# Performance work log

Measured on AMD Instinct MI355X. Metric: run time of the kernel, lower is better.

## Reference

```python
import jax, jax.numpy as jnp
import numpy as np

ETA = 0.1
BETA = 0.1
MU = 0.1
PI_INIT = 0.7
MINI = 1e-6
C_TOTAL = 1e7  # corpus-level token count C[guided_m] (constant scale factor)


def setup_inputs() -> dict:
    key = jax.random.key(0)
    k1, k2, k3, k4, k5, k6 = jax.random.split(key, 6)
    B, V, K, D = 64, 8000, 50, 10000
    batch_BOW = jax.random.randint(k1, (B, V), 0, 3, dtype=jnp.int32)
    batch_indices = jax.random.randint(k2, (B,), 0, D)
    seeds_topic_matrix = (jax.random.uniform(k3, (V, K)) < 0.005).astype(jnp.float32)
    exp_m = jax.random.uniform(k4, (D, K)) * 10.0
    exp_n = jax.random.uniform(k5, (V, K)) * 5.0
    exp_s = jax.random.uniform(k6, (V, K)) * 2.0
    pi = jnp.full((K,), PI_INIT, dtype=jnp.float32)
    return {"batch_BOW": batch_BOW, "batch_indices": batch_indices,
            "seeds_topic_matrix": seeds_topic_matrix, "exp_m": exp_m,
            "exp_n": exp_n, "exp_s": exp_s, "pi": pi, "iter_n": 3}


def reference(batch_BOW, batch_indices, seeds_topic_matrix, exp_m, exp_n, exp_s, pi, iter_n):
    V, K = exp_n.shape
    beta_sum = BETA * V
    seed_word = seeds_topic_matrix.sum(axis=1) > 0          # [V] words that seed any topic
    S = seed_word.astype(exp_s.dtype).sum()
    mu_sum = MU * S
    exp_n_sum = exp_n.sum(axis=0)                            # [K]
    exp_s_sum = exp_s.sum(axis=0)                            # [K]

    bow = batch_BOW.astype(exp_m.dtype)                      # [B,V]
    mask = (bow > 0).astype(exp_m.dtype)[:, :, None]         # [B,V,1] BOW_nonzero gather
    theta = exp_m[batch_indices] + ETA                       # [B,K]

    seed_topic_term = ((MU + exp_s) / (mu_sum + exp_s_sum))[None]       # [1,V,K]
    reg_topic_term = ((BETA + exp_n) / (beta_sum + exp_n_sum))[None]    # [1,V,K]
    seeds_b = seeds_topic_matrix[None]                                   # [1,V,K]
    theta_b = theta[:, None, :]                                          # [B,1,K]

    gamma_ss = mask * seeds_b * theta_b * seed_topic_term * pi
    gamma_sr = mask * seeds_b * theta_b * reg_topic_term * (1.0 - pi)
    gamma_rr = mask * (1.0 - seeds_b) * theta_b * reg_topic_term

    s_sum = (gamma_ss + gamma_sr).sum(-1, keepdims=True)
    r_sum = gamma_rr.sum(-1, keepdims=True)
    gamma_ss = gamma_ss / (s_sum + MINI)
    gamma_sr = gamma_sr / (s_sum + MINI)
    gamma_rr = gamma_rr / (r_sum + MINI)

    # seed words use the mixture; non-seed words use regular-regular responsibilities
    gamma = jnp.where(seed_word[None, :, None],
                      pi * gamma_ss + (1.0 - pi) * (gamma_sr + gamma_rr),
                      gamma_rr)

    temp_exp_m = jnp.einsum('bvk,bv->bk', gamma, bow)
    temp_exp_n = jnp.einsum('bvk,bv->vk', gamma_sr + gamma_rr, bow)
    temp_exp_s = jnp.einsum('bvk,bv->vk', gamma_ss, bow)
    gamma_sr_sum = gamma_sr.sum(axis=(0, 1))
    exp_q_z = jnp.sum(gamma * jnp.log(gamma + MINI))

    rho = 1.0 / float((iter_n + 5) ** 0.9)
    batch_C = bow.sum()
    scale = C_TOTAL / batch_C

    exp_m_batch_new = (1.0 - rho) * exp_m[batch_indices] + rho * temp_exp_m
    exp_s_new = (1.0 - rho) * exp_s + rho * temp_exp_s * scale
    exp_n_new = (1.0 - rho) * exp_n + rho * temp_exp_n * scale

    exp_s_sum_new = exp_s_new.sum(axis=0)
    pi_new = exp_s_sum_new / (exp_s_sum_new + gamma_sr_sum + MINI)
    pi_new = jnp.where(pi_new > 0.1, pi_new, PI_INIT)

    return exp_m_batch_new, exp_n_new, exp_s_new, pi_new, exp_q_z
```

## Files before the change

kernel.cpp:

```cpp
#include <hip/hip_runtime.h>
#include <math.h>

constexpr int Bc = 64;
constexpr int Vc = 8000;
constexpr int Kc = 50;

#define WS_NSUM   0
#define WS_SSUM   50
#define WS_BATCHC 151
#define WS_SCNT   152
#define WS_QZSH   160
#define WS_PM     256
#define WS_GSRSH  51456
#define WS_SSNSH  54656
#define WS_ZEND   56256
#define WS_TH     56256
#define WS_SW     59456
#define WS_END    67456

#define FB_QZ     150
#define FB_GSR    200
#define FB_SSN    256

__global__ __launch_bounds__(256) void k1_pre(const int* __restrict__ bow,
    const float* __restrict__ seeds, const float* __restrict__ exp_n,
    const float* __restrict__ exp_s, const int* __restrict__ bidx,
    const float* __restrict__ exp_m, float* __restrict__ ws)
{
    const int t = threadIdx.x, blk = blockIdx.x;
    if (blk < 100) {
        __shared__ float csn[Kc], css[Kc];
        if (t < Kc) { csn[t] = 0.f; css[t] = 0.f; }
        __syncthreads();
        const int l = t & 63, w = t >> 6;
        const int q = (blk >> 1)*64 + l;
        const int k = q % 50;
        float sn = 0.f, ss = 0.f;
        for (int j = w + (blk & 1)*4; j < 125; j += 8) {
            int flat = j*3200 + q;
            sn += exp_n[flat];
            ss += exp_s[flat];
        }
        atomicAdd(&csn[k], sn);
        atomicAdd(&css[k], ss);
        __syncthreads();
        if (t < Kc) {
            atomicAdd(&ws[WS_NSUM + t], csn[t]);
            atomicAdd(&ws[WS_SSUM + t], css[t]);
        }
    } else if (blk < 164) {
        const int4* b4 = (const int4*)bow;
        int acc = 0;
        for (int i = (blk-100)*256 + t; i < Bc*Vc/4; i += 64*256) {
            int4 x = b4[i];
            acc += x.x + x.y + x.z + x.w;
        }
        for (int off = 32; off; off >>= 1) acc += __shfl_xor(acc, off);
        __shared__ int ri[4];
        if ((t & 63) == 0) ri[t >> 6] = acc;
        __syncthreads();
        if (t == 0) atomicAdd((int*)ws + WS_BATCHC, ri[0]+ri[1]+ri[2]+ri[3]);
    } else if (blk < 196) {
        int v = (blk-164)*256 + t;
        int any = 0;
        if (v < Vc) {
            const float2* rp = (const float2*)(seeds + v*Kc);
            for (int j = 0; j < 25; ++j) {
                float2 x = rp[j];
                any |= (x.x != 0.f) | (x.y != 0.f);
            }
            ws[WS_SW + v] = any ? 1.f : 0.f;
        }
        unsigned long long m = __ballot(any);
        if ((t & 63) == 0) atomicAdd((int*)ws + WS_SCNT, (int)__popcll(m));
    } else {
        for (int i = t; i < Bc*Kc; i += 256) {
            int b = i / Kc, k = i - b*Kc;
            ws[WS_TH + i] = exp_m[bidx[b]*Kc + k] + 0.1f;
        }
    }
}

__global__ __launch_bounds__(256) void kF(const int* __restrict__ bow,
    const float* __restrict__ seeds, const float* __restrict__ exp_n,
    const float* __restrict__ exp_s, const float* __restrict__ pi,
    const int* __restrict__ itern_p, float* __restrict__ ws,
    float* __restrict__ out)
{
    const int id = blockIdx.x;
    const int vt = (id & 7)*63 + (id >> 3);
    if (vt >= Vc/16) return;
    const int v0 = vt * 16;

    __shared__ float  th_l[64*51];
    __shared__ float  pmb[64*51];
    __shared__ float2 cd_l[16*50];
    __shared__ float2 gg_l[16*50];
    __shared__ float  n1_l[16*50];
    __shared__ float2 ii_l[16*64];
    __shared__ unsigned short bow_l[16*64];
    __shared__ float  den_l[152];
    __shared__ float  sw_l[16];
    __shared__ float  qz_l;

    const int t = threadIdx.x, lane = t & 63, w = t >> 6;

    int ii = itern_p[0];
    float itern = (ii >= 0 && ii < 1000000) ? (float)ii : __int_as_float(ii);
    const float rho = 1.f / powf(itern + 5.f, 0.9f);
    const float omr = 1.f - rho;

    for (int i = t; i < Bc*Kc; i += 256) {
        int b = i / 50, k = i - b*50;
        th_l[b*51 + k] = ws[WS_TH + i];
        pmb[b*51 + k]  = 0.f;
    }
    if (t < 50) {
        float Sf = (float)(((const int*)ws)[WS_SCNT]);
        den_l[t] = 1.f / (0.1f*Sf + ws[WS_SSUM + t]);
    } else if (t < 100) {
        den_l[t] = 1.f / (0.1f*(float)Vc + ws[WS_NSUM + t - 50]);
    } else if (t < 150) {
        den_l[t] = pi[t - 100];
    } else if (t >= 160 && t < 176) {
        sw_l[t - 160] = ws[WS_SW + v0 + (t - 160)];
    }
    for (int e = t; e < 16*64; e += 256) {
        int b = e >> 4, vl = e & 15;
        bow_l[vl*64 + b] = (unsigned short)bow[b*Vc + v0 + vl];
    }
    if (t == 0) qz_l = 0.f;
    __syncthreads();

    for (int i = t; i < 16*50; i += 256) {
        int vl = i / 50, k = i - vl*50;
        int g = v0*50 + i;
        float sv = seeds[g], en = exp_n[g], es = exp_s[g];
        float pk = den_l[100 + k];
        float st = (0.1f + es) * den_l[k];
        float rt = (0.1f + en) * den_l[50 + k];
        float sc = sv*st*pk;
        float n1 = sv*rt*(1.f - pk);
        float n2 = (1.f - sv)*rt;
        cd_l[i] = make_float2(sc + n1, n2);
        float ge = fmaf(pk, sc, (1.f - pk)*n1);
        float gf = (sw_l[vl] != 0.f) ? (1.f - pk)*n2 : n2;
        gg_l[i] = make_float2(ge, gf);
        n1_l[i] = n1;
    }
    __syncthreads();

    {
        float pm[Kc];
#pragma unroll
        for (int k = 0; k < Kc; ++k) pm[k] = 0.f;
        float qzacc0 = 0.f, qzacc1 = 0.f;

#pragma unroll 1
        for (int jj = 0; jj < 4; ++jj) {
            const int vl = w*4 + jj;
            const float bw = (float)bow_l[vl*64 + lane];
            const float4* cd4 = (const float4*)(cd_l + vl*50);
            float S = 0.f, S2 = 0.f, R = 0.f, R2 = 0.f;
#pragma unroll 5
            for (int k2 = 0; k2 < 25; ++k2) {
                float th0 = th_l[lane*51 + 2*k2];
                float th1 = th_l[lane*51 + 2*k2 + 1];
                float4 q = cd4[k2];
                S  = fmaf(th0, q.x, S);  R  = fmaf(th0, q.y, R);
                S2 = fmaf(th1, q.z, S2); R2 = fmaf(th1, q.w, R2);
            }
            S += S2; R += R2;
            const bool msk = bw > 0.f;
            const float is = msk ? 1.f/(S + 1e-6f) : 0.f;
            const float ir = msk ? 1.f/(R + 1e-6f) : 0.f;
            ii_l[vl*64 + lane] = make_float2(is, ir);
            const float4* gg4 = (const float4*)(gg_l + vl*50);
#pragma unroll
            for (int k2 = 0; k2 < 25; ++k2) {
                float th0 = th_l[lane*51 + 2*k2];
                float th1 = th_l[lane*51 + 2*k2 + 1];
                float4 q = gg4[k2];
                float t1a = fmaf(q.x, is, q.y*ir);
                float t1b = fmaf(q.z, is, q.w*ir);
                float ga = th0*t1a;
                float gb = th1*t1b;
                qzacc0 = fmaf(ga, __logf(ga + 1e-6f), qzacc0);
                qzacc1 = fmaf(gb, __logf(gb + 1e-6f), qzacc1);
                pm[2*k2]   = fmaf(bw, t1a, pm[2*k2]);
                pm[2*k2+1] = fmaf(bw, t1b, pm[2*k2+1]);
            }
        }

        float qz = qzacc0 + qzacc1;
        for (int off = 32; off; off >>= 1) qz += __shfl_xor(qz, off);
        if (lane == 0) atomicAdd(&qz_l, qz);

        for (int ww = 0; ww < 4; ++ww) {
            if (w == ww) {
#pragma unroll
                for (int k = 0; k < Kc; ++k) pmb[lane*51 + k] += pm[k];
            }
            __syncthreads();
        }
    }

    const int psh = (id & 7)*2 + ((id >> 3) & 1);
    for (int i = t; i < Bc*Kc; i += 256) {
        int b = i / 50, k = i - b*50;
        atomicAdd(&ws[WS_PM + psh*3200 + i], pmb[b*51 + k]);
    }
    if (t == 0) atomicAdd(&ws[WS_QZSH + (id & 31)], qz_l);

    {
        const float bC = (float)(((const int*)ws)[WS_BATCHC]);
        const float rs = rho * (1e7f / bC);
        float PT0=0.f,PT1=0.f,PT2=0.f,PT3=0.f;
        float QT0=0.f,QT1=0.f,QT2=0.f,QT3=0.f;
        float P20=0.f,P21=0.f,P22=0.f,P23=0.f;
#pragma unroll 8
        for (int b = 0; b < Bc; ++b) {
            float thv = th_l[b*51 + lane];
            float2 u0 = ii_l[(w*4+0)*64 + b];
            float2 u1 = ii_l[(w*4+1)*64 + b];
            float2 u2 = ii_l[(w*4+2)*64 + b];
            float2 u3 = ii_l[(w*4+3)*64 + b];
            float b0 = (float)bow_l[(w*4+0)*64 + b];
            float b1 = (float)bow_l[(w*4+1)*64 + b];
            float b2 = (float)bow_l[(w*4+2)*64 + b];
            float b3 = (float)bow_l[(w*4+3)*64 + b];
            PT0 = fmaf(b0*u0.x, thv, PT0); QT0 = fmaf(b0*u0.y, thv, QT0); P20 = fmaf(u0.x, thv, P20);
            PT1 = fmaf(b1*u1.x, thv, PT1); QT1 = fmaf(b1*u1.y, thv, QT1); P21 = fmaf(u1.x, thv, P21);
            PT2 = fmaf(b2*u2.x, thv, PT2); QT2 = fmaf(b2*u2.y, thv, QT2); P22 = fmaf(u2.x, thv, P22);
            PT3 = fmaf(b3*u3.x, thv, PT3); QT3 = fmaf(b3*u3.y, thv, QT3); P23 = fmaf(u3.x, thv, P23);
        }
        if (lane < Kc) {
            float PT[4] = {PT0, PT1, PT2, PT3};
            float QT[4] = {QT0, QT1, QT2, QT3};
            float P2[4] = {P20, P21, P22, P23};
            float gacc = 0.f, ssn = 0.f;
#pragma unroll
            for (int jj = 0; jj < 4; ++jj) {
                const int vl = w*4 + jj;
                const int li = vl*50 + lane;
                const int g  = (v0 + vl)*50 + lane;
                float n1v = n1_l[li];
                float2 cdv = cd_l[li];
                float tn  = fmaf(n1v, PT[jj], cdv.y*QT[jj]);
                float tsv = (cdv.x - n1v)*PT[jj];
                out[3200 + g]          = fmaf(omr, exp_n[g], rs*tn);
                float snew             = fmaf(omr, exp_s[g], rs*tsv);
                out[3200 + 400000 + g] = snew;
                gacc = fmaf(n1v, P2[jj], gacc);
                ssn += snew;
            }
            atomicAdd(&ws[WS_GSRSH + (id & 63)*Kc + lane], gacc);
            atomicAdd(&ws[WS_SSNSH + (id & 31)*Kc + lane], ssn);
        }
    }
}

__global__ __launch_bounds__(256) void kEnd(const int* __restrict__ itern_p,
    float* __restrict__ out, float* __restrict__ ws)
{
    const int t = threadIdx.x, blk = blockIdx.x;
    int ii = itern_p[0];
    float itern = (ii >= 0 && ii < 1000000) ? (float)ii : __int_as_float(ii);
    const float rho = 1.f / powf(itern + 5.f, 0.9f);
    const float omr = 1.f - rho;

    if (blk < 13) {
        int i = blk*256 + t;
        if (i < Bc*Kc) {
            float th = ws[WS_TH + i];
            float pmsum = 0.f;
#pragma unroll
            for (int s = 0; s < 16; ++s) pmsum += ws[WS_PM + s*3200 + i];
            out[i] = fmaf(omr, th - 0.1f, rho*th*pmsum);
        }
    } else {
        if (t < Kc) {
            float ssn = 0.f, srs = 0.f;
#pragma unroll
            for (int s = 0; s < 32; ++s) ssn += ws[WS_SSNSH + s*Kc + t];
#pragma unroll
            for (int s = 0; s < 64; ++s) srs += ws[WS_GSRSH + s*Kc + t];
            float p = ssn / (ssn + srs + 1e-6f);
            out[Bc*Kc + 2*Vc*Kc + t] = (p > 0.1f) ? p : 0.7f;
        }
        if (t == 63) {
            float qz = 0.f;
            for (int s = 0; s < 32; ++s) qz += ws[WS_QZSH + s];
            out[Bc*Kc + 2*Vc*Kc + Kc] = qz;
        }
    }
}

__global__ __launch_bounds__(256) void fb_k1(const int* __restrict__ bow,
    const float* __restrict__ seeds, const float* __restrict__ exp_n,
    const float* __restrict__ exp_s, float* __restrict__ ws)
{
    __shared__ float redf[256];
    __shared__ int   redi[256];
    const int t = threadIdx.x, blk = blockIdx.x;
    if (blk < Kc) {
        float sn = 0.f, ss = 0.f;
        for (int v = t; v < Vc; v += 256) {
            sn += exp_n[v*Kc + blk];
            ss += exp_s[v*Kc + blk];
        }
        redf[t] = sn; __syncthreads();
        for (int s = 128; s > 0; s >>= 1) { if (t < s) redf[t] += redf[t+s]; __syncthreads(); }
        if (t == 0) ws[WS_NSUM + blk] = redf[0];
        __syncthreads();
        redf[t] = ss; __syncthreads();
        for (int s = 128; s > 0; s >>= 1) { if (t < s) redf[t] += redf[t+s]; __syncthreads(); }
        if (t == 0) ws[WS_SSUM + blk] = redf[0];
    } else if (blk < Kc + 32) {
        int acc = 0;
        for (int i = (blk - Kc)*256 + t; i < Bc*Vc; i += 32*256) acc += bow[i];
        redi[t] = acc; __syncthreads();
        for (int s = 128; s > 0; s >>= 1) { if (t < s) redi[t] += redi[t+s]; __syncthreads(); }
        if (t == 0) atomicAdd((int*)ws + WS_BATCHC, redi[0]);
    } else {
        int cnt = 0;
        for (int v = (blk - Kc - 32)*256 + t; v < Vc; v += 8*256) {
            const float* row = seeds + v*Kc;
            int any = 0;
            for (int k = 0; k < Kc; ++k) any |= (row[k] != 0.f);
            cnt += any;
        }
        redi[t] = cnt; __syncthreads();
        for (int s = 128; s > 0; s >>= 1) { if (t < s) redi[t] += redi[t+s]; __syncthreads(); }
        if (t == 0) atomicAdd((int*)ws + WS_SCNT, redi[0]);
    }
}

__global__ __launch_bounds__(512) void fb_k2(
    const int* __restrict__ bow, const int* __restrict__ bidx,
    const float* __restrict__ seeds, const float* __restrict__ exp_m,
    const float* __restrict__ exp_n, const float* __restrict__ exp_s,
    const float* __restrict__ pi, float* __restrict__ ws,
    float* __restrict__ out)
{
    float* out_m = out;
    float* out_n = out + Bc*Kc;
    float* out_s = out + Bc*Kc + Vc*Kc;
    __shared__ float lds_m[Bc*Kc];
    __shared__ float lds_theta[Bc*Kc];
    __shared__ float lds_srsum[Kc];
    __shared__ float lds_qz;
    const int t = threadIdx.x;
    for (int i = t; i < Bc*Kc; i += 512) lds_m[i] = 0.f;
    if (t < Kc) lds_srsum[t] = 0.f;
    if (t == 0) lds_qz = 0.f;
    for (int i = t; i < Bc*Kc; i += 512) {
        int b = i / Kc;
        lds_theta[i] = exp_m[bidx[b]*Kc + (i - b*Kc)] + 0.1f;
    }
    __syncthreads();
    const int lane = t & 63, wid = t >> 6;
    const int gw = blockIdx.x*8 + wid, nw = gridDim.x*8;
    const int k = lane;
    const bool kval = (k < Kc);
    const float S_f = (float)(((const int*)ws)[WS_SCNT]);
    float pi_k = 0.f, omp_k = 0.f, sden_inv = 0.f, rden_inv = 0.f;
    if (kval) {
        pi_k = pi[k]; omp_k = 1.f - pi_k;
        sden_inv = 1.f / (0.1f*S_f + ws[WS_SSUM + k]);
        rden_inv = 1.f / (0.1f*(float)Vc + ws[WS_NSUM + k]);
    }
    float acc_sr = 0.f, acc_qz = 0.f;
    for (int v = gw; v < Vc; v += nw) {
        float seeds_vk = 0.f, es = 0.f, en = 0.f;
        if (kval) { seeds_vk = seeds[v*Kc+k]; es = exp_s[v*Kc+k]; en = exp_n[v*Kc+k]; }
        const float st = (0.1f + es)*sden_inv;
        const float rt = (0.1f + en)*rden_inv;
        const bool seed_word = (__ballot(seeds_vk != 0.f) != 0ULL);
        const float bow_lane = (float)bow[lane*Vc + v];
        float acc_n = 0.f, acc_s = 0.f;
        for (int b = 0; b < Bc; ++b) {
            const float bw = __shfl(bow_lane, b);
            if (bw == 0.f) continue;
            const float th = lds_theta[b*Kc + (kval ? k : 0)];
            float ss = seeds_vk*th*st*pi_k;
            float sr = seeds_vk*th*rt*omp_k;
            float rr = (1.f - seeds_vk)*th*rt;
            float ssum = ss + sr, rsum = rr;
            for (int off = 32; off > 0; off >>= 1) {
                ssum += __shfl_xor(ssum, off);
                rsum += __shfl_xor(rsum, off);
            }
            const float inv_s = __builtin_amdgcn_rcpf(ssum + 1e-6f);
            const float inv_r = __builtin_amdgcn_rcpf(rsum + 1e-6f);
            const float ssn = ss*inv_s, srn = sr*inv_s, rrn = rr*inv_r;
            const float g = seed_word ? (pi_k*ssn + omp_k*(srn + rrn)) : rrn;
            acc_n += (srn + rrn)*bw;
            acc_s += ssn*bw;
            acc_sr += srn;
            acc_qz += g*__logf(g + 1e-6f);
            if (kval) atomicAdd(&lds_m[b*Kc + k], g*bw);
        }
        if (kval) { out_n[v*Kc + k] = acc_n; out_s[v*Kc + k] = acc_s; }
    }
    if (kval) atomicAdd(&lds_srsum[k], acc_sr);
    for (int off = 32; off > 0; off >>= 1) acc_qz += __shfl_xor(acc_qz, off);
    if (lane == 0) atomicAdd(&lds_qz, acc_qz);
    __syncthreads();
    for (int i = t; i < Bc*Kc; i += 512) {
        float vtm = lds_m[i];
        if (vtm != 0.f) atomicAdd(&out_m[i], vtm);
    }
    if (t < Kc) atomicAdd(&ws[FB_GSR + t], lds_srsum[t]);
    if (t == 0) atomicAdd(&ws[FB_QZ], lds_qz);
}

__global__ __launch_bounds__(256) void fb_k3(
    const float* __restrict__ exp_m, const float* __restrict__ exp_n,
    const float* __restrict__ exp_s, const int* __restrict__ bidx,
    const int* __restrict__ itern_p, float* __restrict__ out,
    float* __restrict__ ws)
{
    const int t = threadIdx.x, blk = blockIdx.x;
    int ii = itern_p[0];
    float itern = (ii >= 0 && ii < 1000000) ? (float)ii : __int_as_float(ii);
    const float rho = 1.f / powf(itern + 5.f, 0.9f);
    const float omr = 1.f - rho;
    const float bC = (float)(((const int*)ws)[WS_BATCHC]);
    const float scale = 1e7f / bC;
    float* out_m = out;
    float* out_n = out + Bc*Kc;
    float* out_s = out + Bc*Kc + Vc*Kc;
    if (blk < Kc) {
        const int k = blk;
        float acc = 0.f;
        for (int v = t; v < Vc; v += 256) {
            int i = v*Kc + k;
            out_n[i] = omr*exp_n[i] + rho*scale*out_n[i];
            float snew = omr*exp_s[i] + rho*scale*out_s[i];
            out_s[i] = snew;
            acc += snew;
        }
        __shared__ float redf[256];
        redf[t] = acc; __syncthreads();
        for (int s = 128; s > 0; s >>= 1) { if (t < s) redf[t] += redf[t+s]; __syncthreads(); }
        if (t == 0) atomicAdd(&ws[FB_SSN + k], redf[0]);
    } else {
        for (int i = t; i < Bc*Kc; i += 256) {
            int b = i / Kc;
            out_m[i] = omr*exp_m[bidx[b]*Kc + (i - b*Kc)] + rho*out_m[i];
        }
        if (t == 0) out[Bc*Kc + 2*Vc*Kc + Kc] = ws[FB_QZ];
    }
}

__global__ void fb_k4(const float* __restrict__ ws, float* __restrict__ out) {
    int k = threadIdx.x;
    if (k < Kc) {
        float ssn = ws[FB_SSN + k];
        float srs = ws[FB_GSR + k];
        float p = ssn / (ssn + srs + 1e-6f);
        out[Bc*Kc + 2*Vc*Kc + k] = (p > 0.1f) ? p : 0.7f;
    }
}

extern "C" void kernel_launch(void* const* d_in, const int* in_sizes, int n_in,
                              void* d_out, int out_size, void* d_ws, size_t ws_size,
                              hipStream_t stream)
{
    const int*   bow    = (const int*)d_in[0];
    const int*   bidx   = (const int*)d_in[1];
    const float* seeds  = (const float*)d_in[2];
    const float* exp_m  = (const float*)d_in[3];
    const float* exp_n  = (const float*)d_in[4];
    const float* exp_s  = (const float*)d_in[5];
    const float* pi     = (const float*)d_in[6];
    const int*   iter_n = (const int*)d_in[7];
    float* out = (float*)d_out;
    float* ws  = (float*)d_ws;

    if (ws_size >= (size_t)WS_END * sizeof(float)) {
        hipMemsetAsync(d_ws, 0, WS_ZEND * sizeof(float), stream);
        k1_pre<<<197, 256, 0, stream>>>(bow, seeds, exp_n, exp_s, bidx, exp_m, ws);
        kF<<<504, 256, 0, stream>>>(bow, seeds, exp_n, exp_s, pi, iter_n, ws, out);
        kEnd<<<14, 256, 0, stream>>>(iter_n, out, ws);
    } else {
        size_t zb = 2048;
        if (zb > ws_size) zb = ws_size;
        hipMemsetAsync(d_ws, 0, zb, stream);
        hipMemsetAsync(d_out, 0, Bc*Kc*sizeof(float), stream);
        fb_k1<<<Kc + 32 + 8, 256, 0, stream>>>(bow, seeds, exp_n, exp_s, ws);
        fb_k2<<<256, 512, 0, stream>>>(bow, bidx, seeds, exp_m, exp_n, exp_s, pi, ws, out);
        fb_k3<<<Kc + 1, 256, 0, stream>>>(exp_m, exp_n, exp_s, bidx, iter_n, out, ws);
        fb_k4<<<1, 64, 0, stream>>>(ws, out);
    }
}
```

Before: 52.71 us.

## Double kF block size to 512 threads, two words per wave, atomic LDS merge

The main kernel now launches 512 threads per block, so each of the 8 waves handles 2 of the block's 16 words instead of 4. The per-wave partial theta-update sums are merged into shared memory with LDS atomics instead of a serialized four-step loop with a barrier per step. This is meant to add parallelism within each block, cut per-thread serial work and remove repeated barriers. In exchange, the 512-thread launch bound limits registers per thread, which may cause spills for the 50-element pm array, and there are 50 LDS atomics per thread.

```diff
diff --git a/kernel.cpp b/kernel.cpp
--- a/kernel.cpp
+++ b/kernel.cpp
@@ -81,7 +81,7 @@
     }
 }
 
-__global__ __launch_bounds__(256) void kF(const int* __restrict__ bow,
+__global__ __launch_bounds__(512) void kF(const int* __restrict__ bow,
     const float* __restrict__ seeds, const float* __restrict__ exp_n,
     const float* __restrict__ exp_s, const float* __restrict__ pi,
     const int* __restrict__ itern_p, float* __restrict__ ws,
@@ -110,7 +110,7 @@
     const float rho = 1.f / powf(itern + 5.f, 0.9f);
     const float omr = 1.f - rho;
 
-    for (int i = t; i < Bc*Kc; i += 256) {
+    for (int i = t; i < Bc*Kc; i += 512) {
         int b = i / 50, k = i - b*50;
         th_l[b*51 + k] = ws[WS_TH + i];
         pmb[b*51 + k]  = 0.f;
@@ -125,14 +125,14 @@
     } else if (t >= 160 && t < 176) {
         sw_l[t - 160] = ws[WS_SW + v0 + (t - 160)];
     }
-    for (int e = t; e < 16*64; e += 256) {
+    for (int e = t; e < 16*64; e += 512) {
         int b = e >> 4, vl = e & 15;
         bow_l[vl*64 + b] = (unsigned short)bow[b*Vc + v0 + vl];
     }
     if (t == 0) qz_l = 0.f;
     __syncthreads();
 
-    for (int i = t; i < 16*50; i += 256) {
+    for (int i = t; i < 16*50; i += 512) {
         int vl = i / 50, k = i - vl*50;
         int g = v0*50 + i;
         float sv = seeds[g], en = exp_n[g], es = exp_s[g];
@@ -157,8 +157,8 @@
         float qzacc0 = 0.f, qzacc1 = 0.f;
 
 #pragma unroll 1
-        for (int jj = 0; jj < 4; ++jj) {
-            const int vl = w*4 + jj;
+        for (int jj = 0; jj < 2; ++jj) {
+            const int vl = w*2 + jj;
             const float bw = (float)bow_l[vl*64 + lane];
             const float4* cd4 = (const float4*)(cd_l + vl*50);
             float S = 0.f, S2 = 0.f, R = 0.f, R2 = 0.f;
@@ -196,17 +196,13 @@
         for (int off = 32; off; off >>= 1) qz += __shfl_xor(qz, off);
         if (lane == 0) atomicAdd(&qz_l, qz);
 
-        for (int ww = 0; ww < 4; ++ww) {
-            if (w == ww) {
-#pragma unroll
-                for (int k = 0; k < Kc; ++k) pmb[lane*51 + k] += pm[k];
-            }
-            __syncthreads();
-        }
-    }
+#pragma unroll
+        for (int k = 0; k < Kc; ++k) atomicAdd(&pmb[lane*51 + k], pm[k]);
+    }
+    __syncthreads();
 
     const int psh = (id & 7)*2 + ((id >> 3) & 1);
-    for (int i = t; i < Bc*Kc; i += 256) {
+    for (int i = t; i < Bc*Kc; i += 512) {
         int b = i / 50, k = i - b*50;
         atomicAdd(&ws[WS_PM + psh*3200 + i], pmb[b*51 + k]);
     }
@@ -215,43 +211,44 @@
     {
         const float bC = (float)(((const int*)ws)[WS_BATCHC]);
         const float rs = rho * (1e7f / bC);
-        float PT0=0.f,PT1=0.f,PT2=0.f,PT3=0.f;
-        float QT0=0.f,QT1=0.f,QT2=0.f,QT3=0.f;
-        float P20=0.f,P21=0.f,P22=0.f,P23=0.f;
+        const int vA = w*2, vB = w*2 + 1;
+        float PTa=0.f, QTa=0.f, P2a=0.f, PTb=0.f, QTb=0.f, P2b=0.f;
 #pragma unroll 8
         for (int b = 0; b < Bc; ++b) {
             float thv = th_l[b*51 + lane];
-            float2 u0 = ii_l[(w*4+0)*64 + b];
-            float2 u1 = ii_l[(w*4+1)*64 + b];
-            float2 u2 = ii_l[(w*4+2)*64 + b];
-            float2 u3 = ii_l[(w*4+3)*64 + b];
-            float b0 = (float)bow_l[(w*4+0)*64 + b];
-            float b1 = (float)bow_l[(w*4+1)*64 + b];
-            float b2 = (float)bow_l[(w*4+2)*64 + b];
-            float b3 = (float)bow_l[(w*4+3)*64 + b];
-            PT0 = fmaf(b0*u0.x, thv, PT0); QT0 = fmaf(b0*u0.y, thv, QT0); P20 = fmaf(u0.x, thv, P20);
-            PT1 = fmaf(b1*u1.x, thv, PT1); QT1 = fmaf(b1*u1.y, thv, QT1); P21 = fmaf(u1.x, thv, P21);
-            PT2 = fmaf(b2*u2.x, thv, PT2); QT2 = fmaf(b2*u2.y, thv, QT2); P22 = fmaf(u2.x, thv, P22);
-            PT3 = fmaf(b3*u3.x, thv, PT3); QT3 = fmaf(b3*u3.y, thv, QT3); P23 = fmaf(u3.x, thv, P23);
+            float2 ua = ii_l[vA*64 + b];
+            float2 ub = ii_l[vB*64 + b];
+            float ba = (float)bow_l[vA*64 + b];
+            float bb = (float)bow_l[vB*64 + b];
+            PTa = fmaf(ba*ua.x, thv, PTa); QTa = fmaf(ba*ua.y, thv, QTa); P2a = fmaf(ua.x, thv, P2a);
+            PTb = fmaf(bb*ub.x, thv, PTb); QTb = fmaf(bb*ub.y, thv, QTb); P2b = fmaf(ub.x, thv, P2b);
         }
         if (lane < Kc) {
-            float PT[4] = {PT0, PT1, PT2, PT3};
-            float QT[4] = {QT0, QT1, QT2, QT3};
-            float P2[4] = {P20, P21, P22, P23};
-            float gacc = 0.f, ssn = 0.f;
-#pragma unroll
-            for (int jj = 0; jj < 4; ++jj) {
-                const int vl = w*4 + jj;
-                const int li = vl*50 + lane;
-                const int g  = (v0 + vl)*50 + lane;
+            float gacc, ssn;
+            {
+                const int li = vA*50 + lane;
+                const int g  = (v0 + vA)*50 + lane;
                 float n1v = n1_l[li];
                 float2 cdv = cd_l[li];
-                float tn  = fmaf(n1v, PT[jj], cdv.y*QT[jj]);
-                float tsv = (cdv.x - n1v)*PT[jj];
+                float tn  = fmaf(n1v, PTa, cdv.y*QTa);
+                float tsv = (cdv.x - n1v)*PTa;
                 out[3200 + g]          = fmaf(omr, exp_n[g], rs*tn);
                 float snew             = fmaf(omr, exp_s[g], rs*tsv);
                 out[3200 + 400000 + g] = snew;
-                gacc = fmaf(n1v, P2[jj], gacc);
+                gacc = n1v*P2a;
+                ssn  = snew;
+            }
+            {
+                const int li = vB*50 + lane;
+                const int g  = (v0 + vB)*50 + lane;
+                float n1v = n1_l[li];
+                float2 cdv = cd_l[li];
+                float tn  = fmaf(n1v, PTb, cdv.y*QTb);
+                float tsv = (cdv.x - n1v)*PTb;
+                out[3200 + g]          = fmaf(omr, exp_n[g], rs*tn);
+                float snew             = fmaf(omr, exp_s[g], rs*tsv);
+                out[3200 + 400000 + g] = snew;
+                gacc = fmaf(n1v, P2b, gacc);
                 ssn += snew;
             }
             atomicAdd(&ws[WS_GSRSH + (id & 63)*Kc + lane], gacc);
@@ -482,7 +479,7 @@
     if (ws_size >= (size_t)WS_END * sizeof(float)) {
         hipMemsetAsync(d_ws, 0, WS_ZEND * sizeof(float), stream);
         k1_pre<<<197, 256, 0, stream>>>(bow, seeds, exp_n, exp_s, bidx, exp_m, ws);
-        kF<<<504, 256, 0, stream>>>(bow, seeds, exp_n, exp_s, pi, iter_n, ws, out);
+        kF<<<504, 512, 0, stream>>>(bow, seeds, exp_n, exp_s, pi, iter_n, ws, out);
         kEnd<<<14, 256, 0, stream>>>(iter_n, out, ws);
     } else {
         size_t zb = 2048;
```

Result: slower. 115.4 us (+118.9%).
